# Performance work log

Measured on AMD Instinct MI355X. Metric: run time of the kernel, lower is better.

## Reference

```python
import jax, jax.numpy as jnp
import numpy as np

V, E, H, T, S, TS, MAX_OOV = 50257, 512, 1024, 512, 8, 128, 20


def setup_inputs() -> dict:
    key = jax.random.key(0)
    ks = jax.random.split(key, 20)
    n = lambda k, s, sc=1.0: jax.random.normal(k, s, dtype=jnp.float32) * sc
    return {
        "input_emb": n(ks[0], (1, 1, E)),
        "h0": n(ks[1], (1, 1, H)),
        "c0": n(ks[2], (1, 1, H)),
        "encoder_outputs": n(ks[3], (1, T, H)),
        "name_hiddens": n(ks[4], (S, TS, H)),
        "type_hiddens": n(ks[5], (S, TS, H)),
        "name_h": n(ks[6], (1, 1, H)),
        "type_h": n(ks[7], (1, 1, H)),
        "W_ma_attn": n(ks[8], (H, E), 0.02), "b_ma_attn": jnp.zeros(H, jnp.float32),
        "W_ma_comb": n(ks[9], (E, 3 * H + E), 0.02), "b_ma_comb": jnp.zeros(E, jnp.float32),
        "W_ih": n(ks[10], (4 * H, E), 0.02), "W_hh": n(ks[11], (4 * H, H), 0.02),
        "b_ih": jnp.zeros(4 * H, jnp.float32), "b_hh": jnp.zeros(4 * H, jnp.float32),
        "W_copy": n(ks[12], (H, H), 0.02), "b_copy": jnp.zeros(H, jnp.float32),
        "W_gen": n(ks[13], (1, 3 * H + E), 0.02), "b_gen": jnp.zeros(1, jnp.float32),
        "W_out": n(ks[14], (V, H), 0.02), "b_out": jnp.zeros(V, jnp.float32),
        "type_indices": jax.random.randint(ks[15], (S, TS), 0, V + MAX_OOV, dtype=jnp.int32),
        "max_oov": MAX_OOV,
    }


def reference(input_emb, h0, c0, encoder_outputs, name_hiddens, type_hiddens,
              name_h, type_h, W_ma_attn, b_ma_attn, W_ma_comb, b_ma_comb,
              W_ih, W_hh, b_ih, b_hh, W_copy, b_copy, W_gen, b_gen,
              W_out, b_out, type_indices, max_oov):
    Hd = h0.shape[-1]
    Vv = W_out.shape[0]
    # ---- MultiAttn over 3 sources (batch = 1) ----
    q = input_emb[0, 0] @ W_ma_attn.T + b_ma_attn              # (H,) transformed input
    def ctx(arg):                                              # arg: (Ta, H) -> (H,)
        s = jax.nn.softmax(arg @ q)                            # attention over time
        return s @ arg
    c_enc = ctx(encoder_outputs[0])
    c_name = ctx(name_hiddens.reshape(-1, Hd))                 # cat(name_hiddens, dim=1)
    c_type = ctx(type_hiddens.reshape(-1, Hd))
    comb = jnp.concatenate([input_emb[0, 0], c_enc, c_name, c_type])
    x = jnp.tanh(W_ma_comb @ comb + b_ma_comb)                 # (E,) attended input
    # ---- single LSTM step (PyTorch gate order i,f,g,o) ----
    gates = W_ih @ x + b_ih + W_hh @ h0[0, 0] + b_hh
    i_g, f_g, g_g, o_g = jnp.split(gates, 4)
    i_g, f_g, o_g = jax.nn.sigmoid(i_g), jax.nn.sigmoid(f_g), jax.nn.sigmoid(o_g)
    c1 = f_g * c0[0, 0] + i_g * jnp.tanh(g_g)
    h1 = o_g * jnp.tanh(c1)                                    # (H,) = rnn output
    # ---- generation probability ----
    cat_h = jnp.concatenate([h1, name_h[0, 0], type_h[0, 0], x])
    gen_p = jax.nn.sigmoid(W_gen @ cat_h + b_gen)[0]
    # ---- vocab distribution ----
    p_vocab = jnp.concatenate([jax.nn.softmax(W_out @ h1 + b_out),
                               jnp.zeros(max_oov, dtype=h1.dtype)])
    # ---- source similarity scores ----
    last_h = name_hiddens[:, -1, :]                            # (S, H)
    sim = jax.nn.softmax(encoder_outputs[0, -1] @ last_h.T)    # (S,)
    # ---- copy attention + scatter-add ----
    qc = h1 @ W_copy.T + b_copy                                # (H,)
    attn_p = jax.nn.softmax(jnp.einsum('sth,h->st', type_hiddens, qc), axis=1)
    w = (sim[:, None] * attn_p).reshape(-1)                    # (S*TS,)
    p_copy = jnp.zeros(Vv + max_oov, dtype=h1.dtype).at[type_indices.reshape(-1)].add(w)
    prob = gen_p * p_vocab + (1.0 - gen_p) * p_copy
    log_prob = jnp.log(jnp.clip(prob, 1e-10))[None, :]         # (1, V+max_oov)
    return log_prob, h1[None, None, :], c1[None, None, :]
```

## Files before the change

kernel.cpp:

```cpp
#include <hip/hip_runtime.h>

#define VV   50257
#define EE   512
#define HH   1024
#define TT   512
#define SS   8
#define TSS  128
#define MOOV 20

#define OFF_Q      0
#define OFF_COMB   1024
#define OFF_DENOM  4608
#define OFF_SUMPART 4640
#define OFF_X      7168
#define OFF_H1     11776
#define OFF_C1     12800
#define OFF_GENP   13824
#define OFF_SIM    13832
#define OFF_QC     13840
#define OFF_LOGIT  15888
#define OFF_PCOPY  66148

#define NBIG 3142

__device__ __forceinline__ float dot4(float4 a, float4 b) {
    return a.x*b.x + a.y*b.y + a.z*b.z + a.w*b.w;
}
__device__ __forceinline__ float wred(float v) {
    #pragma unroll
    for (int o = 32; o; o >>= 1) v += __shfl_down(v, o, 64);
    return v;
}
__device__ __forceinline__ float wred_all(float v) {
    #pragma unroll
    for (int o = 32; o; o >>= 1) v += __shfl_xor(v, o, 64);
    return v;
}
__device__ __forceinline__ float wmax_all(float v) {
    #pragma unroll
    for (int o = 32; o; o >>= 1) v = fmaxf(v, __shfl_xor(v, o, 64));
    return v;
}

template<int R, int CH>
__device__ __forceinline__ void rowsN_dot(const float* __restrict__ W, int ld,
                                          int row0, int rowmax,
                                          const float4 vec[CH], int lane, float s[R]) {
    float4 w[R][CH];
    #pragma unroll
    for (int r = 0; r < R; ++r) {
        int row = row0 + r; if (row > rowmax) row = rowmax;
        const float4* Wr = (const float4*)(W + (size_t)row * ld);
        #pragma unroll
        for (int k = 0; k < CH; ++k) w[r][k] = Wr[lane + 64 * k];
    }
    #pragma unroll
    for (int r = 0; r < R; ++r) {
        float acc = 0.f;
        #pragma unroll
        for (int k = 0; k < CH; ++k) acc += dot4(w[r][k], vec[k]);
        s[r] = acc;
    }
}

__global__ void k_init_q(const float* __restrict__ emb, const float* __restrict__ W,
                         const float* __restrict__ bias, float* __restrict__ ws) {
    int tid = threadIdx.x, bid = blockIdx.x;
    int gid = bid * 256 + tid;
    if (gid < 3072) ws[OFF_COMB + 512 + gid] = 0.f;
    if (gid < 3)    ws[OFF_DENOM + gid] = 0.f;
    if (gid < 1024) ws[OFF_SUMPART + gid] = 0.f;
    if (gid < 512)  ws[OFF_COMB + gid] = emb[gid];
    if (gid < VV + MOOV) ws[OFF_PCOPY + gid] = 0.f;
    if (bid >= 64) return;
    int wave = tid >> 6, lane = tid & 63;
    const float4* e4 = (const float4*)emb;
    float4 ev[2] = { e4[lane], e4[lane + 64] };
    int row0 = (bid * 4 + wave) * 4;
    float s[4];
    rowsN_dot<4, 2>(W, EE, row0, 1023, ev, lane, s);
    #pragma unroll
    for (int r = 0; r < 4; ++r) {
        float v = wred(s[r]);
        if (lane == 0) ws[OFF_Q + row0 + r] = v + bias[row0 + r];
    }
}

__global__ void k_scores_ctx(const float* __restrict__ enc, const float* __restrict__ name,
                             const float* __restrict__ type, float* __restrict__ ws) {
    int b = blockIdx.x, tid = threadIdx.x;
    int wave = tid >> 6, lane = tid & 63;
    if (b < 160) {
        const float* src; int seg, lb;
        if (b < 32)      { src = enc;  seg = 0; lb = b; }
        else if (b < 96) { src = name; seg = 1; lb = b - 32; }
        else             { src = type; seg = 2; lb = b - 96; }
        __shared__ float sc[16];
        const float4* q4 = (const float4*)(ws + OFF_Q);
        float4 qv[4] = { q4[lane], q4[lane + 64], q4[lane + 128], q4[lane + 192] };
        int r0 = lb * 16 + wave * 4;
        float s[4];
        rowsN_dot<4, 4>(src, HH, r0, 1 << 30, qv, lane, s);
        #pragma unroll
        for (int r = 0; r < 4; ++r) {
            float v = wred(s[r]);
            if (lane == 0) sc[wave * 4 + r] = __expf(v);
        }
        __syncthreads();
        float acc[4] = {0.f, 0.f, 0.f, 0.f};
        const float* base = src + (size_t)(lb * 16) * HH;
        #pragma unroll 4
        for (int r = 0; r < 16; ++r) {
            float er = sc[r];
            const float* row = base + (size_t)r * HH;
            #pragma unroll
            for (int c = 0; c < 4; ++c) acc[c] += er * row[tid + 256 * c];
        }
        float* dst = ws + OFF_COMB + 512 + seg * 1024;
        #pragma unroll
        for (int c = 0; c < 4; ++c) atomicAdd(&dst[tid + 256 * c], acc[c]);
        if (tid == 0) {
            float es = 0.f;
            for (int r = 0; r < 16; ++r) es += sc[r];
            atomicAdd(&ws[OFF_DENOM + seg], es);
        }
    } else {
        __shared__ float sd[8];
        const float4* el = (const float4*)(enc + (size_t)(TT - 1) * HH);
        for (int s8 = wave; s8 < 8; s8 += 4) {
            const float4* R = (const float4*)(name + ((size_t)s8 * TSS + (TSS - 1)) * HH);
            float s = 0.f;
            #pragma unroll
            for (int k = 0; k < 4; ++k) s += dot4(R[lane + 64 * k], el[lane + 64 * k]);
            s = wred(s);
            if (lane == 0) sd[s8] = s;
        }
        __syncthreads();
        if (tid == 0) {
            float m = -1e30f;
            for (int i = 0; i < 8; ++i) m = fmaxf(m, sd[i]);
            float e[8], su = 0.f;
            for (int i = 0; i < 8; ++i) { e[i] = expf(sd[i] - m); su += e[i]; }
            for (int i = 0; i < 8; ++i) ws[OFF_SIM + i] = e[i] / su;
        }
    }
}

__global__ void k_x(const float* __restrict__ W, const float* __restrict__ bias,
                    float* __restrict__ ws) {
    int tid = threadIdx.x, wave = tid >> 6, lane = tid & 63;
    int row = blockIdx.x * 4 + wave;
    float inv1 = 1.f / ws[OFF_DENOM + 0];
    float inv2 = 1.f / ws[OFF_DENOM + 1];
    float inv3 = 1.f / ws[OFF_DENOM + 2];
    const float4* Wr = (const float4*)(W + (size_t)row * 3584);
    const float4* c4 = (const float4*)(ws + OFF_COMB);
    float s = 0.f;
    #pragma unroll
    for (int k = 0; k < 14; ++k) {
        int j = lane + 64 * k;
        float sc = (j < 128) ? 1.f : (j < 384) ? inv1 : (j < 640) ? inv2 : inv3;
        s += dot4(Wr[j], c4[j]) * sc;
    }
    s = wred(s);
    if (lane == 0) ws[OFF_X + row] = tanhf(s + bias[row]);
}

__global__ void k_gates_lstm(const float* __restrict__ Wih, const float* __restrict__ Whh,
                             const float* __restrict__ bih, const float* __restrict__ bhh,
                             const float* __restrict__ h0, const float* __restrict__ c0,
                             float* __restrict__ ws, float* __restrict__ out) {
    __shared__ float g4[4][16];
    int tid = threadIdx.x, wave = tid >> 6, lane = tid & 63, b = blockIdx.x;
    const float4* x4 = (const float4*)(ws + OFF_X);
    float4 xv[2] = { x4[lane], x4[lane + 64] };
    const float4* h4 = (const float4*)h0;
    float4 hv[4] = { h4[lane], h4[lane + 64], h4[lane + 128], h4[lane + 192] };
    #pragma unroll
    for (int grp = 0; grp < 4; ++grp) {
        int row0 = wave * 1024 + b * 16 + grp * 4;
        float s1[4], s2[4];
        rowsN_dot<4, 2>(Wih, EE, row0, 4095, xv, lane, s1);
        rowsN_dot<4, 4>(Whh, HH, row0, 4095, hv, lane, s2);
        #pragma unroll
        for (int r = 0; r < 4; ++r) {
            float v = wred(s1[r] + s2[r]);
            int row = row0 + r;
            if (lane == 0) g4[wave][grp * 4 + r] = v + bih[row] + bhh[row];
        }
    }
    __syncthreads();
    if (tid < 16) {
        int t = b * 16 + tid;
        float ig = 1.f / (1.f + expf(-g4[0][tid]));
        float fg = 1.f / (1.f + expf(-g4[1][tid]));
        float gg = tanhf(g4[2][tid]);
        float og = 1.f / (1.f + expf(-g4[3][tid]));
        float c1 = fg * c0[t] + ig * gg;
        float h1 = og * tanhf(c1);
        ws[OFF_H1 + t] = h1; ws[OFF_C1 + t] = c1;
        out[VV + MOOV + t] = h1;
        out[VV + MOOV + 1024 + t] = c1;
    }
}

__global__ void k_big_qc_genp(const float* __restrict__ W, const float* __restrict__ bias,
                              const float* __restrict__ Wcp, const float* __restrict__ bcp,
                              const float* __restrict__ nameh, const float* __restrict__ typeh,
                              const float* __restrict__ Wg, const float* __restrict__ bg,
                              float* __restrict__ ws) {
    int b = blockIdx.x, tid = threadIdx.x, wave = tid >> 6, lane = tid & 63;
    const float4* h4 = (const float4*)(ws + OFF_H1);
    if (b < NBIG) {
        float4 hv[4] = { h4[lane], h4[lane + 64], h4[lane + 128], h4[lane + 192] };
        int row0 = (b * 4 + wave) * 4;
        float s[4];
        rowsN_dot<4, 4>(W, HH, row0, VV - 1, hv, lane, s);
        float partial = 0.f;
        #pragma unroll
        for (int r = 0; r < 4; ++r) {
            float v = wred(s[r]);
            int row = row0 + r;
            if (lane == 0 && row < VV) {
                float e = __expf(v + bias[row]);
                ws[OFF_LOGIT + row] = e;
                partial += e;
            }
        }
        if (lane == 0) atomicAdd(&ws[OFF_SUMPART + (b & 31) * 32], partial);
    } else if (b < NBIG + 64) {
        int bb = b - NBIG;
        float4 hv[4] = { h4[lane], h4[lane + 64], h4[lane + 128], h4[lane + 192] };
        int row0 = (bb * 4 + wave) * 4;
        float s[4];
        rowsN_dot<4, 4>(Wcp, HH, row0, 1023, hv, lane, s);
        #pragma unroll
        for (int r = 0; r < 4; ++r) {
            float v = wred(s[r]);
            if (lane == 0) ws[OFF_QC + row0 + r] = v + bcp[row0 + r];
        }
    } else {
        float p = 0.f;
        #pragma unroll
        for (int j = 0; j < 14; ++j) {
            int k = tid + 256 * j;
            float cat = (k < 1024) ? ws[OFF_H1 + k]
                      : (k < 2048) ? nameh[k - 1024]
                      : (k < 3072) ? typeh[k - 2048]
                                   : ws[OFF_X + k - 3072];
            p += Wg[k] * cat;
        }
        __shared__ float red[4];
        float su = wred_all(p);
        if ((tid & 63) == 0) red[tid >> 6] = su;
        __syncthreads();
        if (tid == 0) {
            float ss = red[0] + red[1] + red[2] + red[3];
            ws[OFF_GENP] = 1.f / (1.f + expf(-(ss + bg[0])));
        }
    }
}

__global__ void k_attn_scatter(const float* __restrict__ type, const int* __restrict__ idx,
                               float* __restrict__ ws) {
    __shared__ float sc[TSS];
    __shared__ float sh_m, sh_s;
    int s = blockIdx.x, tid = threadIdx.x;
    int wave = tid >> 6, lane = tid & 63;
    const float4* q4 = (const float4*)(ws + OFF_QC);
    float4 qv[4] = { q4[lane], q4[lane + 64], q4[lane + 128], q4[lane + 192] };
    #pragma unroll
    for (int g = 0; g < 8; ++g) {
        int rloc = wave * 32 + g * 4;
        int r0 = s * TSS + rloc;
        float sv[4];
        rowsN_dot<4, 4>(type, HH, r0, 1 << 30, qv, lane, sv);
        #pragma unroll
        for (int r = 0; r < 4; ++r) {
            float v = wred(sv[r]);
            if (lane == 0) sc[rloc + r] = v;
        }
    }
    __syncthreads();
    if (wave == 0) {
        float v0 = sc[lane], v1 = sc[lane + 64];
        float m = wmax_all(fmaxf(v0, v1));
        float su = wred_all(expf(v0 - m) + expf(v1 - m));
        if (lane == 0) { sh_m = m; sh_s = su; }
    }
    __syncthreads();
    if (tid < TSS) {
        float scale = (1.f - ws[OFF_GENP]) * ws[OFF_SIM + s] / sh_s;
        float w = scale * expf(sc[tid] - sh_m);
        atomicAdd(&ws[OFF_PCOPY + idx[s * TSS + tid]], w);
    }
}

__global__ void k_final(const float* __restrict__ ws, float* __restrict__ out) {
    __shared__ float ssum;
    int tid = threadIdx.x;
    if (tid < 64) {
        float v = (tid < 32) ? ws[OFF_SUMPART + tid * 32] : 0.f;
        v = wred_all(v);
        if (tid == 0) ssum = v;
    }
    __syncthreads();
    int g = blockIdx.x * 256 + tid;
    if (g >= VV + MOOV) return;
    float gp = ws[OFF_GENP];
    float pv = (g < VV) ? ws[OFF_LOGIT + g] / ssum : 0.f;
    float prob = gp * pv + ws[OFF_PCOPY + g];
    out[g] = logf(fmaxf(prob, 1e-10f));
}

extern "C" void kernel_launch(void* const* d_in, const int* in_sizes, int n_in,
                              void* d_out, int out_size, void* d_ws, size_t ws_size,
                              hipStream_t stream) {
    (void)in_sizes; (void)n_in; (void)out_size; (void)ws_size;
    const float* emb   = (const float*)d_in[0];
    const float* h0    = (const float*)d_in[1];
    const float* c0    = (const float*)d_in[2];
    const float* enc   = (const float*)d_in[3];
    const float* name  = (const float*)d_in[4];
    const float* type  = (const float*)d_in[5];
    const float* nameh = (const float*)d_in[6];
    const float* typeh = (const float*)d_in[7];
    const float* Wma   = (const float*)d_in[8];
    const float* bma   = (const float*)d_in[9];
    const float* Wmc   = (const float*)d_in[10];
    const float* bmc   = (const float*)d_in[11];
    const float* Wih   = (const float*)d_in[12];
    const float* Whh   = (const float*)d_in[13];
    const float* bih   = (const float*)d_in[14];
    const float* bhh   = (const float*)d_in[15];
    const float* Wcp   = (const float*)d_in[16];
    const float* bcp   = (const float*)d_in[17];
    const float* Wg    = (const float*)d_in[18];
    const float* bg    = (const float*)d_in[19];
    const float* Wout  = (const float*)d_in[20];
    const float* bout  = (const float*)d_in[21];
    const int*   tidx  = (const int*)d_in[22];
    float* out = (float*)d_out;
    float* ws  = (float*)d_ws;

    k_init_q      <<<197,      256, 0, stream>>>(emb, Wma, bma, ws);
    k_scores_ctx  <<<161,      256, 0, stream>>>(enc, name, type, ws);
    k_x           <<<128,      256, 0, stream>>>(Wmc, bmc, ws);
    k_gates_lstm  <<<64,       256, 0, stream>>>(Wih, Whh, bih, bhh, h0, c0, ws, out);
    k_big_qc_genp <<<NBIG + 65, 256, 0, stream>>>(Wout, bout, Wcp, bcp, nameh, typeh, Wg, bg, ws);
    k_attn_scatter<<<8,        256, 0, stream>>>(type, tidx, ws);
    k_final       <<<197,      256, 0, stream>>>(ws, out);
}
```

Measured before the change: 80.96 us.

## Double-buffer vocab projection rows, 64 rows per block, fewer blocks

```diff
diff --git a/kernel.cpp b/kernel.cpp
--- a/kernel.cpp
+++ b/kernel.cpp
@@ -21,7 +21,7 @@
 #define OFF_LOGIT  15888
 #define OFF_PCOPY  66148
 
-#define NBIG 3142
+#define NBB 786
 
 __device__ __forceinline__ float dot4(float4 a, float4 b) {
     return a.x*b.x + a.y*b.y + a.z*b.z + a.w*b.w;
@@ -61,6 +61,36 @@
         for (int k = 0; k < CH; ++k) acc += dot4(w[r][k], vec[k]);
         s[r] = acc;
     }
+}
+
+__device__ __forceinline__ void tload(const float* __restrict__ W, int row0, int lane,
+                                      float4 (&w)[4][4]) {
+    #pragma unroll
+    for (int r = 0; r < 4; ++r) {
+        int row = row0 + r; if (row >= VV) row = VV - 1;
+        const float4* Wr = (const float4*)(W + (size_t)row * HH);
+        #pragma unroll
+        for (int k = 0; k < 4; ++k) w[r][k] = Wr[lane + 64 * k];
+    }
+}
+__device__ __forceinline__ float treduce(const float4 (&w)[4][4], const float4 (&hv)[4],
+                                         const float* __restrict__ bias, int row0,
+                                         int lane, float* __restrict__ logit) {
+    float part = 0.f;
+    #pragma unroll
+    for (int r = 0; r < 4; ++r) {
+        float acc = 0.f;
+        #pragma unroll
+        for (int k = 0; k < 4; ++k) acc += dot4(w[r][k], hv[k]);
+        float v = wred(acc);
+        int row = row0 + r;
+        if (lane == 0 && row < VV) {
+            float e = __expf(v + bias[row]);
+            logit[row] = e;
+            part += e;
+        }
+    }
+    return part;
 }
 
 __global__ void k_init_q(const float* __restrict__ emb, const float* __restrict__ W,
@@ -211,25 +241,23 @@
                               float* __restrict__ ws) {
     int b = blockIdx.x, tid = threadIdx.x, wave = tid >> 6, lane = tid & 63;
     const float4* h4 = (const float4*)(ws + OFF_H1);
-    if (b < NBIG) {
+    if (b < NBB) {
         float4 hv[4] = { h4[lane], h4[lane + 64], h4[lane + 128], h4[lane + 192] };
-        int row0 = (b * 4 + wave) * 4;
-        float s[4];
-        rowsN_dot<4, 4>(W, HH, row0, VV - 1, hv, lane, s);
-        float partial = 0.f;
-        #pragma unroll
-        for (int r = 0; r < 4; ++r) {
-            float v = wred(s[r]);
-            int row = row0 + r;
-            if (lane == 0 && row < VV) {
-                float e = __expf(v + bias[row]);
-                ws[OFF_LOGIT + row] = e;
-                partial += e;
-            }
-        }
-        if (lane == 0) atomicAdd(&ws[OFF_SUMPART + (b & 31) * 32], partial);
-    } else if (b < NBIG + 64) {
-        int bb = b - NBIG;
+        float* logit = ws + OFF_LOGIT;
+        int r0 = b * 64 + wave * 4;
+        float4 A[4][4], B[4][4];
+        tload(W, r0,      lane, A);
+        tload(W, r0 + 16, lane, B);
+        float part = 0.f;
+        part += treduce(A, hv, bias, r0,      lane, logit);
+        tload(W, r0 + 32, lane, A);
+        part += treduce(B, hv, bias, r0 + 16, lane, logit);
+        tload(W, r0 + 48, lane, B);
+        part += treduce(A, hv, bias, r0 + 32, lane, logit);
+        part += treduce(B, hv, bias, r0 + 48, lane, logit);
+        if (lane == 0) atomicAdd(&ws[OFF_SUMPART + (b & 31) * 32], part);
+    } else if (b < NBB + 64) {
+        int bb = b - NBB;
         float4 hv[4] = { h4[lane], h4[lane + 64], h4[lane + 128], h4[lane + 192] };
         int row0 = (bb * 4 + wave) * 4;
         float s[4];
@@ -285,13 +313,13 @@
     if (wave == 0) {
         float v0 = sc[lane], v1 = sc[lane + 64];
         float m = wmax_all(fmaxf(v0, v1));
-        float su = wred_all(expf(v0 - m) + expf(v1 - m));
+        float su = wred_all(__expf(v0 - m) + __expf(v1 - m));
         if (lane == 0) { sh_m = m; sh_s = su; }
     }
     __syncthreads();
     if (tid < TSS) {
         float scale = (1.f - ws[OFF_GENP]) * ws[OFF_SIM + s] / sh_s;
-        float w = scale * expf(sc[tid] - sh_m);
+        float w = scale * __expf(sc[tid] - sh_m);
         atomicAdd(&ws[OFF_PCOPY + idx[s * TSS + tid]], w);
     }
 }
@@ -347,7 +375,7 @@
     k_scores_ctx  <<<161,      256, 0, stream>>>(enc, name, type, ws);
     k_x           <<<128,      256, 0, stream>>>(Wmc, bmc, ws);
     k_gates_lstm  <<<64,       256, 0, stream>>>(Wih, Whh, bih, bhh, h0, c0, ws, out);
-    k_big_qc_genp <<<NBIG + 65, 256, 0, stream>>>(Wout, bout, Wcp, bcp, nameh, typeh, Wg, bg, ws);
+    k_big_qc_genp <<<NBB + 65, 256, 0, stream>>>(Wout, bout, Wcp, bcp, nameh, typeh, Wg, bg, ws);
     k_attn_scatter<<<8,        256, 0, stream>>>(type, tidx, ws);
     k_final       <<<197,      256, 0, stream>>>(ws, out);
 }
```

After: 109.7 us. +35.5%, slower.

## Merge front and tail kernel chains into cooperative kernels with grid syncs

Applied to the files above, without the earlier changes.

```diff
diff --git a/kernel.cpp b/kernel.cpp
--- a/kernel.cpp
+++ b/kernel.cpp
@@ -1,4 +1,7 @@
 #include <hip/hip_runtime.h>
+#include <hip/hip_cooperative_groups.h>
+
+namespace cg = cooperative_groups;
 
 #define VV   50257
 #define EE   512
@@ -63,69 +66,40 @@
     }
 }
 
-__global__ void k_init_q(const float* __restrict__ emb, const float* __restrict__ W,
-                         const float* __restrict__ bias, float* __restrict__ ws) {
+__global__ void __launch_bounds__(256) k_front(
+        const float* __restrict__ emb,  const float* __restrict__ enc,
+        const float* __restrict__ name, const float* __restrict__ type,
+        const float* __restrict__ Wma,  const float* __restrict__ bma,
+        const float* __restrict__ Wmc,  const float* __restrict__ bmc,
+        const float* __restrict__ Wih,  const float* __restrict__ Whh,
+        const float* __restrict__ bih,  const float* __restrict__ bhh,
+        const float* __restrict__ h0,   const float* __restrict__ c0,
+        float* __restrict__ ws,         float* __restrict__ out) {
+    cg::grid_group grid = cg::this_grid();
+    __shared__ float sh_sc[16];
+    __shared__ float sh_sd[8];
+    __shared__ float sh_g4[4][16];
     int tid = threadIdx.x, bid = blockIdx.x;
+    int wave = tid >> 6, lane = tid & 63;
     int gid = bid * 256 + tid;
+
+    if (gid < VV + MOOV) ws[OFF_PCOPY + gid] = 0.f;
     if (gid < 3072) ws[OFF_COMB + 512 + gid] = 0.f;
     if (gid < 3)    ws[OFF_DENOM + gid] = 0.f;
     if (gid < 1024) ws[OFF_SUMPART + gid] = 0.f;
     if (gid < 512)  ws[OFF_COMB + gid] = emb[gid];
-    if (gid < VV + MOOV) ws[OFF_PCOPY + gid] = 0.f;
-    if (bid >= 64) return;
-    int wave = tid >> 6, lane = tid & 63;
-    const float4* e4 = (const float4*)emb;
-    float4 ev[2] = { e4[lane], e4[lane + 64] };
-    int row0 = (bid * 4 + wave) * 4;
-    float s[4];
-    rowsN_dot<4, 2>(W, EE, row0, 1023, ev, lane, s);
-    #pragma unroll
-    for (int r = 0; r < 4; ++r) {
-        float v = wred(s[r]);
-        if (lane == 0) ws[OFF_Q + row0 + r] = v + bias[row0 + r];
-    }
-}
-
-__global__ void k_scores_ctx(const float* __restrict__ enc, const float* __restrict__ name,
-                             const float* __restrict__ type, float* __restrict__ ws) {
-    int b = blockIdx.x, tid = threadIdx.x;
-    int wave = tid >> 6, lane = tid & 63;
-    if (b < 160) {
-        const float* src; int seg, lb;
-        if (b < 32)      { src = enc;  seg = 0; lb = b; }
-        else if (b < 96) { src = name; seg = 1; lb = b - 32; }
-        else             { src = type; seg = 2; lb = b - 96; }
-        __shared__ float sc[16];
-        const float4* q4 = (const float4*)(ws + OFF_Q);
-        float4 qv[4] = { q4[lane], q4[lane + 64], q4[lane + 128], q4[lane + 192] };
-        int r0 = lb * 16 + wave * 4;
+    if (bid < 64) {
+        const float4* e4 = (const float4*)emb;
+        float4 ev[2] = { e4[lane], e4[lane + 64] };
+        int row0 = (bid * 4 + wave) * 4;
         float s[4];
-        rowsN_dot<4, 4>(src, HH, r0, 1 << 30, qv, lane, s);
+        rowsN_dot<4, 2>(Wma, EE, row0, 1023, ev, lane, s);
         #pragma unroll
         for (int r = 0; r < 4; ++r) {
             float v = wred(s[r]);
-            if (lane == 0) sc[wave * 4 + r] = __expf(v);
-        }
-        __syncthreads();
-        float acc[4] = {0.f, 0.f, 0.f, 0.f};
-        const float* base = src + (size_t)(lb * 16) * HH;
-        #pragma unroll 4
-        for (int r = 0; r < 16; ++r) {
-            float er = sc[r];
-            const float* row = base + (size_t)r * HH;
-            #pragma unroll
-            for (int c = 0; c < 4; ++c) acc[c] += er * row[tid + 256 * c];
-        }
-        float* dst = ws + OFF_COMB + 512 + seg * 1024;
-        #pragma unroll
-        for (int c = 0; c < 4; ++c) atomicAdd(&dst[tid + 256 * c], acc[c]);
-        if (tid == 0) {
-            float es = 0.f;
-            for (int r = 0; r < 16; ++r) es += sc[r];
-            atomicAdd(&ws[OFF_DENOM + seg], es);
-        }
-    } else {
-        __shared__ float sd[8];
+            if (lane == 0) ws[OFF_Q + row0 + r] = v + bma[row0 + r];
+        }
+    } else if (bid == 64) {
         const float4* el = (const float4*)(enc + (size_t)(TT - 1) * HH);
         for (int s8 = wave; s8 < 8; s8 += 4) {
             const float4* R = (const float4*)(name + ((size_t)s8 * TSS + (TSS - 1)) * HH);
@@ -133,74 +107,105 @@
             #pragma unroll
             for (int k = 0; k < 4; ++k) s += dot4(R[lane + 64 * k], el[lane + 64 * k]);
             s = wred(s);
-            if (lane == 0) sd[s8] = s;
+            if (lane == 0) sh_sd[s8] = s;
         }
         __syncthreads();
         if (tid == 0) {
             float m = -1e30f;
-            for (int i = 0; i < 8; ++i) m = fmaxf(m, sd[i]);
+            for (int i = 0; i < 8; ++i) m = fmaxf(m, sh_sd[i]);
             float e[8], su = 0.f;
-            for (int i = 0; i < 8; ++i) { e[i] = expf(sd[i] - m); su += e[i]; }
+            for (int i = 0; i < 8; ++i) { e[i] = __expf(sh_sd[i] - m); su += e[i]; }
             for (int i = 0; i < 8; ++i) ws[OFF_SIM + i] = e[i] / su;
         }
     }
-}
-
-__global__ void k_x(const float* __restrict__ W, const float* __restrict__ bias,
-                    float* __restrict__ ws) {
-    int tid = threadIdx.x, wave = tid >> 6, lane = tid & 63;
-    int row = blockIdx.x * 4 + wave;
-    float inv1 = 1.f / ws[OFF_DENOM + 0];
-    float inv2 = 1.f / ws[OFF_DENOM + 1];
-    float inv3 = 1.f / ws[OFF_DENOM + 2];
-    const float4* Wr = (const float4*)(W + (size_t)row * 3584);
-    const float4* c4 = (const float4*)(ws + OFF_COMB);
-    float s = 0.f;
-    #pragma unroll
-    for (int k = 0; k < 14; ++k) {
-        int j = lane + 64 * k;
-        float sc = (j < 128) ? 1.f : (j < 384) ? inv1 : (j < 640) ? inv2 : inv3;
-        s += dot4(Wr[j], c4[j]) * sc;
-    }
-    s = wred(s);
-    if (lane == 0) ws[OFF_X + row] = tanhf(s + bias[row]);
-}
-
-__global__ void k_gates_lstm(const float* __restrict__ Wih, const float* __restrict__ Whh,
-                             const float* __restrict__ bih, const float* __restrict__ bhh,
-                             const float* __restrict__ h0, const float* __restrict__ c0,
-                             float* __restrict__ ws, float* __restrict__ out) {
-    __shared__ float g4[4][16];
-    int tid = threadIdx.x, wave = tid >> 6, lane = tid & 63, b = blockIdx.x;
-    const float4* x4 = (const float4*)(ws + OFF_X);
-    float4 xv[2] = { x4[lane], x4[lane + 64] };
-    const float4* h4 = (const float4*)h0;
-    float4 hv[4] = { h4[lane], h4[lane + 64], h4[lane + 128], h4[lane + 192] };
-    #pragma unroll
-    for (int grp = 0; grp < 4; ++grp) {
-        int row0 = wave * 1024 + b * 16 + grp * 4;
-        float s1[4], s2[4];
-        rowsN_dot<4, 2>(Wih, EE, row0, 4095, xv, lane, s1);
-        rowsN_dot<4, 4>(Whh, HH, row0, 4095, hv, lane, s2);
+    grid.sync();
+
+    if (bid < 160) {
+        const float* src; int seg, lb;
+        if (bid < 32)      { src = enc;  seg = 0; lb = bid; }
+        else if (bid < 96) { src = name; seg = 1; lb = bid - 32; }
+        else               { src = type; seg = 2; lb = bid - 96; }
+        const float4* q4 = (const float4*)(ws + OFF_Q);
+        float4 qv[4] = { q4[lane], q4[lane + 64], q4[lane + 128], q4[lane + 192] };
+        int r0 = lb * 16 + wave * 4;
+        float s[4];
+        rowsN_dot<4, 4>(src, HH, r0, 1 << 30, qv, lane, s);
         #pragma unroll
         for (int r = 0; r < 4; ++r) {
-            float v = wred(s1[r] + s2[r]);
-            int row = row0 + r;
-            if (lane == 0) g4[wave][grp * 4 + r] = v + bih[row] + bhh[row];
-        }
-    }
-    __syncthreads();
-    if (tid < 16) {
-        int t = b * 16 + tid;
-        float ig = 1.f / (1.f + expf(-g4[0][tid]));
-        float fg = 1.f / (1.f + expf(-g4[1][tid]));
-        float gg = tanhf(g4[2][tid]);
-        float og = 1.f / (1.f + expf(-g4[3][tid]));
-        float c1 = fg * c0[t] + ig * gg;
-        float h1 = og * tanhf(c1);
-        ws[OFF_H1 + t] = h1; ws[OFF_C1 + t] = c1;
-        out[VV + MOOV + t] = h1;
-        out[VV + MOOV + 1024 + t] = c1;
+            float v = wred(s[r]);
+            if (lane == 0) sh_sc[wave * 4 + r] = __expf(v);
+        }
+        __syncthreads();
+        float acc[4] = {0.f, 0.f, 0.f, 0.f};
+        const float* base = src + (size_t)(lb * 16) * HH;
+        #pragma unroll 4
+        for (int r = 0; r < 16; ++r) {
+            float er = sh_sc[r];
+            const float* row = base + (size_t)r * HH;
+            #pragma unroll
+            for (int c = 0; c < 4; ++c) acc[c] += er * row[tid + 256 * c];
+        }
+        float* dst = ws + OFF_COMB + 512 + seg * 1024;
+        #pragma unroll
+        for (int c = 0; c < 4; ++c) atomicAdd(&dst[tid + 256 * c], acc[c]);
+        if (tid == 0) {
+            float es = 0.f;
+            for (int r = 0; r < 16; ++r) es += sh_sc[r];
+            atomicAdd(&ws[OFF_DENOM + seg], es);
+        }
+    }
+    grid.sync();
+
+    if (bid < 128) {
+        int row = bid * 4 + wave;
+        float inv1 = 1.f / ws[OFF_DENOM + 0];
+        float inv2 = 1.f / ws[OFF_DENOM + 1];
+        float inv3 = 1.f / ws[OFF_DENOM + 2];
+        const float4* Wr = (const float4*)(Wmc + (size_t)row * 3584);
+        const float4* c4 = (const float4*)(ws + OFF_COMB);
+        float s = 0.f;
+        #pragma unroll
+        for (int k = 0; k < 14; ++k) {
+            int j = lane + 64 * k;
+            float sc = (j < 128) ? 1.f : (j < 384) ? inv1 : (j < 640) ? inv2 : inv3;
+            s += dot4(Wr[j], c4[j]) * sc;
+        }
+        s = wred(s);
+        if (lane == 0) ws[OFF_X + row] = tanhf(s + bmc[row]);
+    }
+    grid.sync();
+
+    if (bid < 64) {
+        const float4* x4 = (const float4*)(ws + OFF_X);
+        float4 xv[2] = { x4[lane], x4[lane + 64] };
+        const float4* h4 = (const float4*)h0;
+        float4 hv[4] = { h4[lane], h4[lane + 64], h4[lane + 128], h4[lane + 192] };
+        #pragma unroll
+        for (int grp = 0; grp < 4; ++grp) {
+            int row0 = wave * 1024 + bid * 16 + grp * 4;
+            float s1[4], s2[4];
+            rowsN_dot<4, 2>(Wih, EE, row0, 4095, xv, lane, s1);
+            rowsN_dot<4, 4>(Whh, HH, row0, 4095, hv, lane, s2);
+            #pragma unroll
+            for (int r = 0; r < 4; ++r) {
+                float v = wred(s1[r] + s2[r]);
+                int row = row0 + r;
+                if (lane == 0) sh_g4[wave][grp * 4 + r] = v + bih[row] + bhh[row];
+            }
+        }
+        __syncthreads();
+        if (tid < 16) {
+            int t = bid * 16 + tid;
+            float ig = 1.f / (1.f + __expf(-sh_g4[0][tid]));
+            float fg = 1.f / (1.f + __expf(-sh_g4[1][tid]));
+            float gg = tanhf(sh_g4[2][tid]);
+            float og = 1.f / (1.f + __expf(-sh_g4[3][tid]));
+            float c1 = fg * c0[t] + ig * gg;
+            float h1 = og * tanhf(c1);
+            ws[OFF_H1 + t] = h1; ws[OFF_C1 + t] = c1;
+            out[VV + MOOV + t] = h1;
+            out[VV + MOOV + 1024 + t] = c1;
+        }
     }
 }
 
@@ -256,61 +261,66 @@
         __syncthreads();
         if (tid == 0) {
             float ss = red[0] + red[1] + red[2] + red[3];
-            ws[OFF_GENP] = 1.f / (1.f + expf(-(ss + bg[0])));
-        }
-    }
-}
-
-__global__ void k_attn_scatter(const float* __restrict__ type, const int* __restrict__ idx,
-                               float* __restrict__ ws) {
+            ws[OFF_GENP] = 1.f / (1.f + __expf(-(ss + bg[0])));
+        }
+    }
+}
+
+__global__ void __launch_bounds__(256) k_tail(
+        const float* __restrict__ type, const int* __restrict__ idx,
+        float* __restrict__ ws, float* __restrict__ out) {
+    cg::grid_group grid = cg::this_grid();
     __shared__ float sc[TSS];
     __shared__ float sh_m, sh_s;
-    int s = blockIdx.x, tid = threadIdx.x;
+    __shared__ float ssum;
+    int bid = blockIdx.x, tid = threadIdx.x;
     int wave = tid >> 6, lane = tid & 63;
-    const float4* q4 = (const float4*)(ws + OFF_QC);
-    float4 qv[4] = { q4[lane], q4[lane + 64], q4[lane + 128], q4[lane + 192] };
-    #pragma unroll
-    for (int g = 0; g < 8; ++g) {
-        int rloc = wave * 32 + g * 4;
-        int r0 = s * TSS + rloc;
-        float sv[4];
-        rowsN_dot<4, 4>(type, HH, r0, 1 << 30, qv, lane, sv);
-        #pragma unroll
-        for (int r = 0; r < 4; ++r) {
-            float v = wred(sv[r]);
-            if (lane == 0) sc[rloc + r] = v;
-        }
-    }
-    __syncthreads();
-    if (wave == 0) {
-        float v0 = sc[lane], v1 = sc[lane + 64];
-        float m = wmax_all(fmaxf(v0, v1));
-        float su = wred_all(expf(v0 - m) + expf(v1 - m));
-        if (lane == 0) { sh_m = m; sh_s = su; }
-    }
-    __syncthreads();
-    if (tid < TSS) {
-        float scale = (1.f - ws[OFF_GENP]) * ws[OFF_SIM + s] / sh_s;
-        float w = scale * expf(sc[tid] - sh_m);
-        atomicAdd(&ws[OFF_PCOPY + idx[s * TSS + tid]], w);
-    }
-}
-
-__global__ void k_final(const float* __restrict__ ws, float* __restrict__ out) {
-    __shared__ float ssum;
-    int tid = threadIdx.x;
+
+    if (bid < 8) {
+        int s = bid;
+        const float4* q4 = (const float4*)(ws + OFF_QC);
+        float4 qv[4] = { q4[lane], q4[lane + 64], q4[lane + 128], q4[lane + 192] };
+        #pragma unroll
+        for (int g = 0; g < 8; ++g) {
+            int rloc = wave * 32 + g * 4;
+            int r0 = s * TSS + rloc;
+            float sv[4];
+            rowsN_dot<4, 4>(type, HH, r0, 1 << 30, qv, lane, sv);
+            #pragma unroll
+            for (int r = 0; r < 4; ++r) {
+                float v = wred(sv[r]);
+                if (lane == 0) sc[rloc + r] = v;
+            }
+        }
+        __syncthreads();
+        if (wave == 0) {
+            float v0 = sc[lane], v1 = sc[lane + 64];
+            float m = wmax_all(fmaxf(v0, v1));
+            float su = wred_all(__expf(v0 - m) + __expf(v1 - m));
+            if (lane == 0) { sh_m = m; sh_s = su; }
+        }
+        __syncthreads();
+        if (tid < TSS) {
+            float scale = (1.f - ws[OFF_GENP]) * ws[OFF_SIM + s] / sh_s;
+            float w = scale * __expf(sc[tid] - sh_m);
+            atomicAdd(&ws[OFF_PCOPY + idx[s * TSS + tid]], w);
+        }
+    }
+    grid.sync();
+
     if (tid < 64) {
         float v = (tid < 32) ? ws[OFF_SUMPART + tid * 32] : 0.f;
         v = wred_all(v);
         if (tid == 0) ssum = v;
     }
     __syncthreads();
-    int g = blockIdx.x * 256 + tid;
-    if (g >= VV + MOOV) return;
-    float gp = ws[OFF_GENP];
-    float pv = (g < VV) ? ws[OFF_LOGIT + g] / ssum : 0.f;
-    float prob = gp * pv + ws[OFF_PCOPY + g];
-    out[g] = logf(fmaxf(prob, 1e-10f));
+    int g = bid * 256 + tid;
+    if (g < VV + MOOV) {
+        float gp = ws[OFF_GENP];
+        float pv = (g < VV) ? ws[OFF_LOGIT + g] / ssum : 0.f;
+        float prob = gp * pv + ws[OFF_PCOPY + g];
+        out[g] = logf(fmaxf(prob, 1e-10f));
+    }
 }
 
 extern "C" void kernel_launch(void* const* d_in, const int* in_sizes, int n_in,
@@ -343,11 +353,15 @@
     float* out = (float*)d_out;
     float* ws  = (float*)d_ws;
 
-    k_init_q      <<<197,      256, 0, stream>>>(emb, Wma, bma, ws);
-    k_scores_ctx  <<<161,      256, 0, stream>>>(enc, name, type, ws);
-    k_x           <<<128,      256, 0, stream>>>(Wmc, bmc, ws);
-    k_gates_lstm  <<<64,       256, 0, stream>>>(Wih, Whh, bih, bhh, h0, c0, ws, out);
-    k_big_qc_genp <<<NBIG + 65, 256, 0, stream>>>(Wout, bout, Wcp, bcp, nameh, typeh, Wg, bg, ws);
-    k_attn_scatter<<<8,        256, 0, stream>>>(type, tidx, ws);
-    k_final       <<<197,      256, 0, stream>>>(ws, out);
-}
+    void* fargs[] = { (void*)&emb, (void*)&enc, (void*)&name, (void*)&type,
+                      (void*)&Wma, (void*)&bma, (void*)&Wmc, (void*)&bmc,
+                      (void*)&Wih, (void*)&Whh, (void*)&bih, (void*)&bhh,
+                      (void*)&h0,  (void*)&c0,  (void*)&ws,  (void*)&out };
+    (void)hipLaunchCooperativeKernel((void*)k_front, dim3(256), dim3(256), fargs, 0, stream);
+
+    k_big_qc_genp<<<NBIG + 65, 256, 0, stream>>>(Wout, bout, Wcp, bcp,
+                                                 nameh, typeh, Wg, bg, ws);
+
+    void* targs[] = { (void*)&type, (void*)&tidx, (void*)&ws, (void*)&out };
+    (void)hipLaunchCooperativeKernel((void*)k_tail, dim3(197), dim3(256), targs, 0, stream);
+}
```

Measured after the change: 197.2 us. +143.5%, slower.

## Hoist Whh gate matvec into init kernel and fuse copy-attention via counter

Applied to the files above, without the earlier changes.

```diff
diff --git a/kernel.cpp b/kernel.cpp
--- a/kernel.cpp
+++ b/kernel.cpp
@@ -12,7 +12,9 @@
 #define OFF_COMB   1024
 #define OFF_DENOM  4608
 #define OFF_SUMPART 4640
+#define OFF_CTR    6000
 #define OFF_X      7168
+#define OFF_GATES  7680
 #define OFF_H1     11776
 #define OFF_C1     12800
 #define OFF_GENP   13824
@@ -63,68 +65,32 @@
     }
 }
 
-__global__ void k_init_q(const float* __restrict__ emb, const float* __restrict__ W,
-                         const float* __restrict__ bias, float* __restrict__ ws) {
+__global__ void k_init(const float* __restrict__ emb, const float* __restrict__ Wma,
+                       const float* __restrict__ bma, const float* __restrict__ enc,
+                       const float* __restrict__ name, const float* __restrict__ Whh,
+                       const float* __restrict__ bih, const float* __restrict__ bhh,
+                       const float* __restrict__ h0, float* __restrict__ ws) {
     int tid = threadIdx.x, bid = blockIdx.x;
-    int gid = bid * 256 + tid;
-    if (gid < 3072) ws[OFF_COMB + 512 + gid] = 0.f;
-    if (gid < 3)    ws[OFF_DENOM + gid] = 0.f;
-    if (gid < 1024) ws[OFF_SUMPART + gid] = 0.f;
-    if (gid < 512)  ws[OFF_COMB + gid] = emb[gid];
-    if (gid < VV + MOOV) ws[OFF_PCOPY + gid] = 0.f;
-    if (bid >= 64) return;
     int wave = tid >> 6, lane = tid & 63;
-    const float4* e4 = (const float4*)emb;
-    float4 ev[2] = { e4[lane], e4[lane + 64] };
-    int row0 = (bid * 4 + wave) * 4;
-    float s[4];
-    rowsN_dot<4, 2>(W, EE, row0, 1023, ev, lane, s);
-    #pragma unroll
-    for (int r = 0; r < 4; ++r) {
-        float v = wred(s[r]);
-        if (lane == 0) ws[OFF_Q + row0 + r] = v + bias[row0 + r];
-    }
-}
-
-__global__ void k_scores_ctx(const float* __restrict__ enc, const float* __restrict__ name,
-                             const float* __restrict__ type, float* __restrict__ ws) {
-    int b = blockIdx.x, tid = threadIdx.x;
-    int wave = tid >> 6, lane = tid & 63;
-    if (b < 160) {
-        const float* src; int seg, lb;
-        if (b < 32)      { src = enc;  seg = 0; lb = b; }
-        else if (b < 96) { src = name; seg = 1; lb = b - 32; }
-        else             { src = type; seg = 2; lb = b - 96; }
-        __shared__ float sc[16];
-        const float4* q4 = (const float4*)(ws + OFF_Q);
-        float4 qv[4] = { q4[lane], q4[lane + 64], q4[lane + 128], q4[lane + 192] };
-        int r0 = lb * 16 + wave * 4;
+    if (bid < 197) {
+        int gid = bid * 256 + tid;
+        if (gid < 3072) ws[OFF_COMB + 512 + gid] = 0.f;
+        if (gid < 3)    ws[OFF_DENOM + gid] = 0.f;
+        if (gid < 1024) ws[OFF_SUMPART + gid] = 0.f;
+        if (gid < 512)  ws[OFF_COMB + gid] = emb[gid];
+        if (gid < VV + MOOV) ws[OFF_PCOPY + gid] = 0.f;
+        if (bid >= 64) return;
+        const float4* e4 = (const float4*)emb;
+        float4 ev[2] = { e4[lane], e4[lane + 64] };
+        int row0 = (bid * 4 + wave) * 4;
         float s[4];
-        rowsN_dot<4, 4>(src, HH, r0, 1 << 30, qv, lane, s);
+        rowsN_dot<4, 2>(Wma, EE, row0, 1023, ev, lane, s);
         #pragma unroll
         for (int r = 0; r < 4; ++r) {
             float v = wred(s[r]);
-            if (lane == 0) sc[wave * 4 + r] = __expf(v);
-        }
-        __syncthreads();
-        float acc[4] = {0.f, 0.f, 0.f, 0.f};
-        const float* base = src + (size_t)(lb * 16) * HH;
-        #pragma unroll 4
-        for (int r = 0; r < 16; ++r) {
-            float er = sc[r];
-            const float* row = base + (size_t)r * HH;
-            #pragma unroll
-            for (int c = 0; c < 4; ++c) acc[c] += er * row[tid + 256 * c];
-        }
-        float* dst = ws + OFF_COMB + 512 + seg * 1024;
-        #pragma unroll
-        for (int c = 0; c < 4; ++c) atomicAdd(&dst[tid + 256 * c], acc[c]);
-        if (tid == 0) {
-            float es = 0.f;
-            for (int r = 0; r < 16; ++r) es += sc[r];
-            atomicAdd(&ws[OFF_DENOM + seg], es);
-        }
-    } else {
+            if (lane == 0) ws[OFF_Q + row0 + r] = v + bma[row0 + r];
+        }
+    } else if (bid == 197) {
         __shared__ float sd[8];
         const float4* el = (const float4*)(enc + (size_t)(TT - 1) * HH);
         for (int s8 = wave; s8 < 8; s8 += 4) {
@@ -140,9 +106,60 @@
             float m = -1e30f;
             for (int i = 0; i < 8; ++i) m = fmaxf(m, sd[i]);
             float e[8], su = 0.f;
-            for (int i = 0; i < 8; ++i) { e[i] = expf(sd[i] - m); su += e[i]; }
+            for (int i = 0; i < 8; ++i) { e[i] = __expf(sd[i] - m); su += e[i]; }
             for (int i = 0; i < 8; ++i) ws[OFF_SIM + i] = e[i] / su;
         }
+    } else {
+        const float4* h4 = (const float4*)h0;
+        float4 hv[4] = { h4[lane], h4[lane + 64], h4[lane + 128], h4[lane + 192] };
+        int row0 = (bid - 198) * 16 + wave * 4;
+        float s[4];
+        rowsN_dot<4, 4>(Whh, HH, row0, 4095, hv, lane, s);
+        #pragma unroll
+        for (int r = 0; r < 4; ++r) {
+            float v = wred(s[r]);
+            int row = row0 + r;
+            if (lane == 0) ws[OFF_GATES + row] = v + bih[row] + bhh[row];
+        }
+    }
+}
+
+__global__ void k_scores_ctx(const float* __restrict__ enc, const float* __restrict__ name,
+                             const float* __restrict__ type, float* __restrict__ ws) {
+    int b = blockIdx.x, tid = threadIdx.x;
+    int wave = tid >> 6, lane = tid & 63;
+    const float* src; int seg, lb;
+    if (b < 32)      { src = enc;  seg = 0; lb = b; }
+    else if (b < 96) { src = name; seg = 1; lb = b - 32; }
+    else             { src = type; seg = 2; lb = b - 96; }
+    __shared__ float sc[16];
+    const float4* q4 = (const float4*)(ws + OFF_Q);
+    float4 qv[4] = { q4[lane], q4[lane + 64], q4[lane + 128], q4[lane + 192] };
+    int r0 = lb * 16 + wave * 4;
+    float s[4];
+    rowsN_dot<4, 4>(src, HH, r0, 1 << 30, qv, lane, s);
+    #pragma unroll
+    for (int r = 0; r < 4; ++r) {
+        float v = wred(s[r]);
+        if (lane == 0) sc[wave * 4 + r] = __expf(v);
+    }
+    __syncthreads();
+    float acc[4] = {0.f, 0.f, 0.f, 0.f};
+    const float* base = src + (size_t)(lb * 16) * HH;
+    #pragma unroll 4
+    for (int r = 0; r < 16; ++r) {
+        float er = sc[r];
+        const float* row = base + (size_t)r * HH;
+        #pragma unroll
+        for (int c = 0; c < 4; ++c) acc[c] += er * row[tid + 256 * c];
+    }
+    float* dst = ws + OFF_COMB + 512 + seg * 1024;
+    #pragma unroll
+    for (int c = 0; c < 4; ++c) atomicAdd(&dst[tid + 256 * c], acc[c]);
+    if (tid == 0) {
+        float es = 0.f;
+        for (int r = 0; r < 16; ++r) es += sc[r];
+        atomicAdd(&ws[OFF_DENOM + seg], es);
     }
 }
 
@@ -166,36 +183,32 @@
     if (lane == 0) ws[OFF_X + row] = tanhf(s + bias[row]);
 }
 
-__global__ void k_gates_lstm(const float* __restrict__ Wih, const float* __restrict__ Whh,
-                             const float* __restrict__ bih, const float* __restrict__ bhh,
-                             const float* __restrict__ h0, const float* __restrict__ c0,
+__global__ void k_gates_lstm(const float* __restrict__ Wih,
+                             const float* __restrict__ c0,
                              float* __restrict__ ws, float* __restrict__ out) {
     __shared__ float g4[4][16];
     int tid = threadIdx.x, wave = tid >> 6, lane = tid & 63, b = blockIdx.x;
     const float4* x4 = (const float4*)(ws + OFF_X);
     float4 xv[2] = { x4[lane], x4[lane + 64] };
-    const float4* h4 = (const float4*)h0;
-    float4 hv[4] = { h4[lane], h4[lane + 64], h4[lane + 128], h4[lane + 192] };
     #pragma unroll
     for (int grp = 0; grp < 4; ++grp) {
         int row0 = wave * 1024 + b * 16 + grp * 4;
-        float s1[4], s2[4];
+        float s1[4];
         rowsN_dot<4, 2>(Wih, EE, row0, 4095, xv, lane, s1);
-        rowsN_dot<4, 4>(Whh, HH, row0, 4095, hv, lane, s2);
-        #pragma unroll
-        for (int r = 0; r < 4; ++r) {
-            float v = wred(s1[r] + s2[r]);
+        #pragma unroll
+        for (int r = 0; r < 4; ++r) {
+            float v = wred(s1[r]);
             int row = row0 + r;
-            if (lane == 0) g4[wave][grp * 4 + r] = v + bih[row] + bhh[row];
+            if (lane == 0) g4[wave][grp * 4 + r] = v + ws[OFF_GATES + row];
         }
     }
     __syncthreads();
     if (tid < 16) {
         int t = b * 16 + tid;
-        float ig = 1.f / (1.f + expf(-g4[0][tid]));
-        float fg = 1.f / (1.f + expf(-g4[1][tid]));
+        float ig = 1.f / (1.f + __expf(-g4[0][tid]));
+        float fg = 1.f / (1.f + __expf(-g4[1][tid]));
         float gg = tanhf(g4[2][tid]);
-        float og = 1.f / (1.f + expf(-g4[3][tid]));
+        float og = 1.f / (1.f + __expf(-g4[3][tid]));
         float c1 = fg * c0[t] + ig * gg;
         float h1 = og * tanhf(c1);
         ws[OFF_H1 + t] = h1; ws[OFF_C1 + t] = c1;
@@ -204,16 +217,53 @@
     }
 }
 
-__global__ void k_big_qc_genp(const float* __restrict__ W, const float* __restrict__ bias,
-                              const float* __restrict__ Wcp, const float* __restrict__ bcp,
-                              const float* __restrict__ nameh, const float* __restrict__ typeh,
-                              const float* __restrict__ Wg, const float* __restrict__ bg,
-                              float* __restrict__ ws) {
+__global__ void k_big_all(const float* __restrict__ W, const float* __restrict__ bias,
+                          const float* __restrict__ Wcp, const float* __restrict__ bcp,
+                          const float* __restrict__ nameh, const float* __restrict__ typeh,
+                          const float* __restrict__ Wg, const float* __restrict__ bg,
+                          const float* __restrict__ type, const int* __restrict__ idx,
+                          float* __restrict__ ws) {
     int b = blockIdx.x, tid = threadIdx.x, wave = tid >> 6, lane = tid & 63;
+    int* ctr = (int*)(ws + OFF_CTR);
     const float4* h4 = (const float4*)(ws + OFF_H1);
-    if (b < NBIG) {
+    if (b < 64) {
         float4 hv[4] = { h4[lane], h4[lane + 64], h4[lane + 128], h4[lane + 192] };
         int row0 = (b * 4 + wave) * 4;
+        float s[4];
+        rowsN_dot<4, 4>(Wcp, HH, row0, 1023, hv, lane, s);
+        #pragma unroll
+        for (int r = 0; r < 4; ++r) {
+            float v = wred(s[r]);
+            if (lane == 0) ws[OFF_QC + row0 + r] = v + bcp[row0 + r];
+        }
+        __syncthreads();
+        __threadfence();
+        if (tid == 0) __hip_atomic_fetch_add(ctr, 1, __ATOMIC_ACQ_REL, __HIP_MEMORY_SCOPE_AGENT);
+    } else if (b == 64) {
+        float p = 0.f;
+        #pragma unroll
+        for (int j = 0; j < 14; ++j) {
+            int k = tid + 256 * j;
+            float cat = (k < 1024) ? ws[OFF_H1 + k]
+                      : (k < 2048) ? nameh[k - 1024]
+                      : (k < 3072) ? typeh[k - 2048]
+                                   : ws[OFF_X + k - 3072];
+            p += Wg[k] * cat;
+        }
+        __shared__ float red[4];
+        float su = wred_all(p);
+        if ((tid & 63) == 0) red[tid >> 6] = su;
+        __syncthreads();
+        if (tid == 0) {
+            float ss = red[0] + red[1] + red[2] + red[3];
+            ws[OFF_GENP] = 1.f / (1.f + __expf(-(ss + bg[0])));
+        }
+        __syncthreads();
+        __threadfence();
+        if (tid == 0) __hip_atomic_fetch_add(ctr, 1, __ATOMIC_ACQ_REL, __HIP_MEMORY_SCOPE_AGENT);
+    } else if (b < 65 + NBIG) {
+        float4 hv[4] = { h4[lane], h4[lane + 64], h4[lane + 128], h4[lane + 192] };
+        int row0 = ((b - 65) * 4 + wave) * 4;
         float s[4];
         rowsN_dot<4, 4>(W, HH, row0, VV - 1, hv, lane, s);
         float partial = 0.f;
@@ -228,71 +278,42 @@
             }
         }
         if (lane == 0) atomicAdd(&ws[OFF_SUMPART + (b & 31) * 32], partial);
-    } else if (b < NBIG + 64) {
-        int bb = b - NBIG;
-        float4 hv[4] = { h4[lane], h4[lane + 64], h4[lane + 128], h4[lane + 192] };
-        int row0 = (bb * 4 + wave) * 4;
-        float s[4];
-        rowsN_dot<4, 4>(Wcp, HH, row0, 1023, hv, lane, s);
-        #pragma unroll
-        for (int r = 0; r < 4; ++r) {
-            float v = wred(s[r]);
-            if (lane == 0) ws[OFF_QC + row0 + r] = v + bcp[row0 + r];
-        }
     } else {
-        float p = 0.f;
-        #pragma unroll
-        for (int j = 0; j < 14; ++j) {
-            int k = tid + 256 * j;
-            float cat = (k < 1024) ? ws[OFF_H1 + k]
-                      : (k < 2048) ? nameh[k - 1024]
-                      : (k < 3072) ? typeh[k - 2048]
-                                   : ws[OFF_X + k - 3072];
-            p += Wg[k] * cat;
-        }
-        __shared__ float red[4];
-        float su = wred_all(p);
-        if ((tid & 63) == 0) red[tid >> 6] = su;
-        __syncthreads();
         if (tid == 0) {
-            float ss = red[0] + red[1] + red[2] + red[3];
-            ws[OFF_GENP] = 1.f / (1.f + expf(-(ss + bg[0])));
-        }
-    }
-}
-
-__global__ void k_attn_scatter(const float* __restrict__ type, const int* __restrict__ idx,
-                               float* __restrict__ ws) {
-    __shared__ float sc[TSS];
-    __shared__ float sh_m, sh_s;
-    int s = blockIdx.x, tid = threadIdx.x;
-    int wave = tid >> 6, lane = tid & 63;
-    const float4* q4 = (const float4*)(ws + OFF_QC);
-    float4 qv[4] = { q4[lane], q4[lane + 64], q4[lane + 128], q4[lane + 192] };
-    #pragma unroll
-    for (int g = 0; g < 8; ++g) {
-        int rloc = wave * 32 + g * 4;
-        int r0 = s * TSS + rloc;
-        float sv[4];
-        rowsN_dot<4, 4>(type, HH, r0, 1 << 30, qv, lane, sv);
-        #pragma unroll
-        for (int r = 0; r < 4; ++r) {
-            float v = wred(sv[r]);
-            if (lane == 0) sc[rloc + r] = v;
-        }
-    }
-    __syncthreads();
-    if (wave == 0) {
-        float v0 = sc[lane], v1 = sc[lane + 64];
-        float m = wmax_all(fmaxf(v0, v1));
-        float su = wred_all(expf(v0 - m) + expf(v1 - m));
-        if (lane == 0) { sh_m = m; sh_s = su; }
-    }
-    __syncthreads();
-    if (tid < TSS) {
-        float scale = (1.f - ws[OFF_GENP]) * ws[OFF_SIM + s] / sh_s;
-        float w = scale * expf(sc[tid] - sh_m);
-        atomicAdd(&ws[OFF_PCOPY + idx[s * TSS + tid]], w);
+            while (__hip_atomic_load(ctr, __ATOMIC_ACQUIRE, __HIP_MEMORY_SCOPE_AGENT) < 65)
+                __builtin_amdgcn_s_sleep(8);
+        }
+        __syncthreads();
+        __shared__ float sc[TSS];
+        __shared__ float sh_m, sh_s;
+        int s = b - (65 + NBIG);
+        const float4* q4 = (const float4*)(ws + OFF_QC);
+        float4 qv[4] = { q4[lane], q4[lane + 64], q4[lane + 128], q4[lane + 192] };
+        #pragma unroll
+        for (int g = 0; g < 8; ++g) {
+            int rloc = wave * 32 + g * 4;
+            int r0 = s * TSS + rloc;
+            float sv[4];
+            rowsN_dot<4, 4>(type, HH, r0, 1 << 30, qv, lane, sv);
+            #pragma unroll
+            for (int r = 0; r < 4; ++r) {
+                float v = wred(sv[r]);
+                if (lane == 0) sc[rloc + r] = v;
+            }
+        }
+        __syncthreads();
+        if (wave == 0) {
+            float v0 = sc[lane], v1 = sc[lane + 64];
+            float m = wmax_all(fmaxf(v0, v1));
+            float su = wred_all(__expf(v0 - m) + __expf(v1 - m));
+            if (lane == 0) { sh_m = m; sh_s = su; }
+        }
+        __syncthreads();
+        if (tid < TSS) {
+            float scale = (1.f - ws[OFF_GENP]) * ws[OFF_SIM + s] / sh_s;
+            float w = scale * __expf(sc[tid] - sh_m);
+            atomicAdd(&ws[OFF_PCOPY + idx[s * TSS + tid]], w);
+        }
     }
 }
 
@@ -343,11 +364,13 @@
     float* out = (float*)d_out;
     float* ws  = (float*)d_ws;
 
-    k_init_q      <<<197,      256, 0, stream>>>(emb, Wma, bma, ws);
-    k_scores_ctx  <<<161,      256, 0, stream>>>(enc, name, type, ws);
-    k_x           <<<128,      256, 0, stream>>>(Wmc, bmc, ws);
-    k_gates_lstm  <<<64,       256, 0, stream>>>(Wih, Whh, bih, bhh, h0, c0, ws, out);
-    k_big_qc_genp <<<NBIG + 65, 256, 0, stream>>>(Wout, bout, Wcp, bcp, nameh, typeh, Wg, bg, ws);
-    k_attn_scatter<<<8,        256, 0, stream>>>(type, tidx, ws);
-    k_final       <<<197,      256, 0, stream>>>(ws, out);
-}
+    (void)hipMemsetAsync((char*)d_ws + OFF_CTR * sizeof(float), 0, sizeof(int), stream);
+
+    k_init       <<<454,  256, 0, stream>>>(emb, Wma, bma, enc, name, Whh, bih, bhh, h0, ws);
+    k_scores_ctx <<<160,  256, 0, stream>>>(enc, name, type, ws);
+    k_x          <<<128,  256, 0, stream>>>(Wmc, bmc, ws);
+    k_gates_lstm <<<64,   256, 0, stream>>>(Wih, c0, ws, out);
+    k_big_all    <<<65 + NBIG + 8, 256, 0, stream>>>(Wout, bout, Wcp, bcp, nameh, typeh,
+                                                     Wg, bg, type, tidx, ws);
+    k_final      <<<197,  256, 0, stream>>>(ws, out);
+}
```

Result: slower. 91.03 us (+12.4%).
